# Optimization experiments

Measured on AMD Instinct MI355X. Metric: run time of the kernel, lower is better.

Reference implementation:

```python
import jax, jax.numpy as jnp
import numpy as np
import math

B, S, D, H = 2, 2048, 1024, 16
DH = D // H
PHI = (1 + math.sqrt(5)) / 2

def _carrier_phases(n_heads):
    # DimensionalHeadManager: 7 rungs with weights 1/phi^i, base phases k*pi/7,
    # per-rung heads spread uniformly around the circle.
    base = [k * math.pi / 7 for k in range(7)]
    raw_w = [1.0 / PHI ** i for i in range(7)]
    tw = sum(raw_w)
    alloc = [max(1, round(n_heads * w / tw)) for w in raw_w]
    while sum(alloc) > n_heads:
        alloc[alloc.index(max(alloc))] -= 1
    while sum(alloc) < n_heads:
        alloc[alloc.index(max(alloc))] += 1
    phases = []
    for r, c in enumerate(alloc):
        for j in range(c):
            phases.append(base[r] + 2 * math.pi / max(c, 1) * j)
    return np.array(phases, dtype=np.float32)

def setup_inputs() -> dict:
    key = jax.random.key(0)
    ks = jax.random.split(key, 8)
    x = jax.random.normal(ks[0], (B, S, D), dtype=jnp.float32)
    input_phase = jax.random.uniform(ks[1], (B, S), dtype=jnp.float32) * (2 * math.pi)
    sc = 1.0 / math.sqrt(D)
    Wq = jax.random.normal(ks[2], (D, D), dtype=jnp.float32) * sc
    Wk = jax.random.normal(ks[3], (D, D), dtype=jnp.float32) * sc
    Wv = jax.random.normal(ks[4], (D, D), dtype=jnp.float32) * sc
    Wo = jax.random.normal(ks[5], (D, D), dtype=jnp.float32) * sc
    gamma = jnp.ones((D,), dtype=jnp.float32)
    beta = jnp.zeros((D,), dtype=jnp.float32)
    # per-head fractal compression exponents > 1 (sub-linear for |x|<1)
    exponents = 1.0 + 0.5 * jax.random.uniform(ks[6], (H,), dtype=jnp.float32)
    carrier_phases = jnp.asarray(_carrier_phases(H))
    balance = jnp.asarray(0.5, dtype=jnp.float32)  # BALANCE
    return {"x": x, "input_phase": input_phase, "Wq": Wq, "Wk": Wk, "Wv": Wv,
            "Wo": Wo, "gamma": gamma, "beta": beta, "exponents": exponents,
            "carrier_phases": carrier_phases, "balance": balance}

def _layernorm(x, gamma, beta, eps=1e-5):
    mu = jnp.mean(x, axis=-1, keepdims=True)
    var = jnp.var(x, axis=-1, keepdims=True)
    return (x - mu) * jax.lax.rsqrt(var + eps) * gamma + beta

def _fractal_compress(kv, exps):
    # sign-preserving power-law compression, per-head exponent
    sign = jnp.sign(kv)
    mag = jnp.maximum(jnp.abs(kv), 1e-8)
    return sign * mag ** exps  # exps broadcast (1,H,1,1)

def reference(x, input_phase, Wq, Wk, Wv, Wo, gamma, beta, exponents,
              carrier_phases, balance):
    h = _layernorm(x, gamma, beta)
    def split_heads(t):
        return t.reshape(B, S, H, DH).transpose(0, 2, 1, 3)  # (B,H,S,dh)
    q = split_heads(h @ Wq)
    k = split_heads(h @ Wk)
    v = split_heads(h @ Wv)
    exps = exponents.reshape(1, H, 1, 1)
    k_c = _fractal_compress(k, exps)
    v_c = _fractal_compress(v, exps)
    # per-head carrier resonance: (B,S,H) in [0,1]
    T = jnp.cos((input_phase[:, :, None] - carrier_phases[None, None, :]) / 2.0) ** 2
    Th = T.transpose(0, 2, 1)  # (B,H,S)
    # balance temperature tau = clip(1/(2*balance), 0.1, 10)
    tau = jnp.clip(1.0 / (2.0 * balance + 1e-8), 0.1, 10.0)
    scores = jnp.einsum('bhqd,bhkd->bhqk', q, k_c) / math.sqrt(DH)
    # phase modulation: key-side resonance enters scores in log-space
    scores = scores + jnp.log(Th[:, :, None, :] + 1e-6)
    causal = jnp.tril(jnp.ones((S, S), dtype=bool))
    scores = jnp.where(causal[None, None], scores, jnp.float32(-1e9))
    attn = jax.nn.softmax(scores / tau, axis=-1)
    out = jnp.einsum('bhqk,bhkd->bhqd', attn, v_c)
    # query-side resonance gates the per-head output
    out = out * Th[:, :, :, None]
    out = out.transpose(0, 2, 1, 3).reshape(B, S, D)
    return x + out @ Wo
```

## Files before the change

### kernel.cpp

```cpp
#include <hip/hip_runtime.h>
#include <math.h>

namespace {
constexpr int B = 2, S = 2048, D = 1024, H = 16, DH = 64;
constexpr int BH = B * H;
constexpr int BS = B * S;
constexpr size_t MAT = (size_t)BS * D;
constexpr int QT = S / 64;
}

typedef __attribute__((ext_vector_type(8))) short s16x8;
typedef __attribute__((ext_vector_type(4))) short s16x4;
typedef __attribute__((ext_vector_type(4))) float f32x4;

__device__ inline unsigned short f2bf(float f) {
  union { float f; unsigned u; } c; c.f = f;
  unsigned r = c.u + 0x7fffu + ((c.u >> 16) & 1u);
  return (unsigned short)(r >> 16);
}
__device__ inline short f2bft(float f) {
  union { float f; unsigned u; } c; c.f = f;
  return (short)((c.u + 0x8000u) >> 16);
}
__device__ inline float bf2f(short s) {
  union { unsigned u; float f; } c;
  c.u = ((unsigned)(unsigned short)s) << 16;
  return c.f;
}
__device__ inline void gld16(const unsigned short* g, unsigned short* l) {
  __builtin_amdgcn_global_load_lds(
      (const __attribute__((address_space(1))) unsigned int*)g,
      (__attribute__((address_space(3))) unsigned int*)l, 16, 0, 0);
}

__global__ __launch_bounds__(256) void k_prep(
    const float* __restrict__ x, const float* __restrict__ gamma,
    const float* __restrict__ beta, unsigned short* __restrict__ h,
    const float* __restrict__ phase, const float* __restrict__ cp,
    const float* __restrict__ bal, float* __restrict__ Th,
    float* __restrict__ Lt, const float* __restrict__ W0,
    const float* __restrict__ W1, const float* __restrict__ W2,
    const float* __restrict__ W3, unsigned short* __restrict__ T0,
    unsigned short* __restrict__ T1, unsigned short* __restrict__ T2,
    unsigned short* __restrict__ T3) {
  __shared__ float shbuf[32 * 33];
  int id = blockIdx.x;
  int t = threadIdx.x;
  if (id < 4096) {
    int z = id & 3;
    int bx = ((id >> 2) & 31) * 32;
    int by = (id >> 7) * 32;
    const float* W = (z == 0) ? W0 : (z == 1) ? W1 : (z == 2) ? W2 : W3;
    unsigned short* T = (z == 0) ? T0 : (z == 1) ? T1 : (z == 2) ? T2 : T3;
    int tc = t & 31, tr = t >> 5;
    float(*tile)[33] = (float(*)[33])shbuf;
#pragma unroll
    for (int i = 0; i < 4; i++)
      tile[tr + 8 * i][tc] = W[(size_t)(by + tr + 8 * i) * D + bx + tc];
    __syncthreads();
#pragma unroll
    for (int i = 0; i < 4; i++)
      T[(size_t)(bx + tr + 8 * i) * D + by + tc] = f2bf(tile[tc][tr + 8 * i]);
  } else if (id < 8192) {
    int row = id - 4096;
    float* red = shbuf;
    const float* xr = x + (size_t)row * D;
    float v[4];
    float s = 0.f;
#pragma unroll
    for (int i = 0; i < 4; i++) {
      v[i] = xr[t + 256 * i];
      s += v[i];
    }
    red[t] = s;
    __syncthreads();
    for (int off = 128; off > 0; off >>= 1) {
      if (t < off) red[t] += red[t + off];
      __syncthreads();
    }
    float mu = red[0] * (1.0f / D);
    __syncthreads();
    float s2 = 0.f;
#pragma unroll
    for (int i = 0; i < 4; i++) {
      float d0 = v[i] - mu;
      s2 += d0 * d0;
    }
    red[t] = s2;
    __syncthreads();
    for (int off = 128; off > 0; off >>= 1) {
      if (t < off) red[t] += red[t + off];
      __syncthreads();
    }
    float r = rsqrtf(red[0] * (1.0f / D) + 1e-5f);
    unsigned short* hr = h + (size_t)row * D;
#pragma unroll
    for (int i = 0; i < 4; i++) {
      int c = t + 256 * i;
      hr[c] = f2bf((v[i] - mu) * r * gamma[c] + beta[c]);
    }
  } else {
    int idx = (id - 8192) * 256 + t;
    int s = idx & (S - 1);
    int bh = idx >> 11;
    int hh = bh & (H - 1);
    int b = bh >> 4;
    float tau = fminf(fmaxf(1.0f / (2.0f * bal[0] + 1e-8f), 0.1f), 10.0f);
    float c = cosf((phase[b * S + s] - cp[hh]) * 0.5f);
    float T = c * c;
    Th[idx] = T;
    Lt[idx] = __log2f(T + 1e-6f) * (1.0f / tau);
  }
}

#define MFMA_GEMM_LOOP_TBUF(AP, BP)                                           \
  do {                                                                        \
    gld16(AP, &As[0][chunkA][0]);                                             \
    gld16(AP + (size_t)16 * D, &As[0][chunkA + 16][0]);                       \
    gld16(BP, &Bs[0][chunkA][0]);                                             \
    gld16(BP + (size_t)16 * D, &Bs[0][chunkA + 16][0]);                       \
    gld16(AP + 32, &As[1][chunkA][0]);                                        \
    gld16(AP + (size_t)16 * D + 32, &As[1][chunkA + 16][0]);                  \
    gld16(BP + 32, &Bs[1][chunkA][0]);                                        \
    gld16(BP + (size_t)16 * D + 32, &Bs[1][chunkA + 16][0]);                  \
    int cur = 0;                                                              \
    for (int k0 = 0; k0 < D; k0 += 32) {                                      \
      if (k0 + 32 < D)                                                        \
        asm volatile("s_waitcnt vmcnt(4)" ::: "memory");                      \
      else                                                                    \
        asm volatile("s_waitcnt vmcnt(0)" ::: "memory");                      \
      asm volatile("s_barrier" ::: "memory");                                 \
      if (k0 + 64 < D) {                                                      \
        int nxt = (cur >= 1) ? cur - 1 : 2;                    \
        gld16(AP + k0 + 64, &As[nxt][chunkA][0]);                             \
        gld16(AP + (size_t)16 * D + k0 + 64, &As[nxt][chunkA + 16][0]);       \
        gld16(BP + k0 + 64, &Bs[nxt][chunkA][0]);                             \
        gld16(BP + (size_t)16 * D + k0 + 64, &Bs[nxt][chunkA + 16][0]);       \
      }                                                                       \
      s16x8 af[4], bf[4];                                                     \
      _Pragma("unroll") for (int i = 0; i < 4; i++) {                         \
        af[i] = *(const s16x8*)&As[cur][wm + i * 16 + lane16][quad * 8];      \
        bf[i] = *(const s16x8*)&Bs[cur][wn + i * 16 + lane16][quad * 8];      \
      }                                                                       \
      _Pragma("unroll") for (int i = 0; i < 4; i++)                           \
          _Pragma("unroll") for (int j = 0; j < 4; j++) acc[i][j] =           \
          __builtin_amdgcn_mfma_f32_16x16x32_bf16(af[i], bf[j], acc[i][j],    \
                                                  0, 0, 0);                   \
      cur = (cur == 2) ? 0 : cur + 1;                                         \
    }                                                                         \
  } while (0)

__global__ __launch_bounds__(256) void k_gemm_qkvv(
    const unsigned short* __restrict__ hm, const unsigned short* __restrict__ Wq,
    const unsigned short* __restrict__ Wk, const unsigned short* __restrict__ Wv,
    const float* __restrict__ exps, unsigned short* __restrict__ q,
    unsigned short* __restrict__ kc, unsigned short* __restrict__ vt) {
  __shared__ __align__(16) unsigned short As[3][128][32];
  __shared__ __align__(16) unsigned short Bs[3][128][32];
  int id = blockIdx.x;
  int xcd = id & 7;
  int inner = id >> 3;
  int z = inner >> 5;
  int rem = inner & 31;
  int mt = (xcd >> 1) * 8 + (rem >> 2);
  int nt = (xcd & 1) * 4 + (rem & 3);
  const unsigned short *Ap, *Bp;
  int tileM, tileN;
  if (z < 2) {
    Ap = hm; Bp = (z == 0) ? Wq : Wk;
    tileM = mt * 128; tileN = nt * 128;
  } else {
    Ap = Wv; Bp = hm;
    tileM = nt * 128; tileN = mt * 128;
  }
  int t = threadIdx.x;
  int wave = t >> 6, lane = t & 63, lane16 = lane & 15, quad = lane >> 4;
  int wm = (wave >> 1) * 64, wn = (wave & 1) * 64;
  int chunkA = wave * 32;
  int srow = (lane >> 2), scol = (lane & 3) * 8;
  const unsigned short* aptr = Ap + (size_t)(tileM + chunkA + srow) * D + scol;
  const unsigned short* bptr = Bp + (size_t)(tileN + chunkA + srow) * D + scol;
  f32x4 acc[4][4] = {};
  MFMA_GEMM_LOOP_TBUF(aptr, bptr);
  if (z < 2) {
    unsigned short* __restrict__ outp = (z == 0) ? q : kc;
    float e0 = exps[tileN >> 6];
    float e1 = exps[(tileN >> 6) + 1];
#pragma unroll
    for (int i = 0; i < 4; i++) {
#pragma unroll
      for (int r = 0; r < 4; r++) {
        int row = tileM + wm + i * 16 + quad * 4 + r;
        int b = row >> 11, s = row & (S - 1);
#pragma unroll
        for (int j = 0; j < 4; j++) {
          int cloc = wn + j * 16 + lane16;
          int head = (tileN + cloc) >> 6;
          int dh = cloc & 63;
          float val = acc[i][j][r];
          if (z != 0) {
            float e = (cloc >> 6) ? e1 : e0;
            float sgn = (val > 0.f) ? 1.f : ((val < 0.f) ? -1.f : 0.f);
            float mg = fmaxf(fabsf(val), 1e-8f);
            val = sgn * __expf(e * __logf(mg));
          }
          outp[((size_t)(b * H + head) * S + s) * DH + dh] = f2bf(val);
        }
      }
    }
  } else {
#pragma unroll
    for (int i = 0; i < 4; i++) {
#pragma unroll
      for (int r = 0; r < 4; r++) {
        int m = tileM + wm + i * 16 + quad * 4 + r;
        int head = m >> 6, dh = m & 63;
        float e = exps[head];
#pragma unroll
        for (int j = 0; j < 4; j++) {
          int n = tileN + wn + j * 16 + lane16;
          int b = n >> 11, s = n & (S - 1);
          float val = acc[i][j][r];
          float sgn = (val > 0.f) ? 1.f : ((val < 0.f) ? -1.f : 0.f);
          float mg = fmaxf(fabsf(val), 1e-8f);
          val = sgn * __expf(e * __logf(mg));
          vt[((size_t)(b * H + head) * DH + dh) * S + s] = f2bf(val);
        }
      }
    }
  }
}

__global__ __launch_bounds__(256) void k_gemm_out_mfma(
    const unsigned short* __restrict__ am, const unsigned short* __restrict__ Wt,
    const float* __restrict__ x, float* __restrict__ outp) {
  __shared__ __align__(16) unsigned short As[3][128][32];
  __shared__ __align__(16) unsigned short Bs[3][128][32];
  int id = blockIdx.x;
  int xcd = id & 7;
  int inner = id >> 3;
  int tileM = ((xcd >> 1) * 8 + (inner >> 2)) * 128;
  int tileN = ((xcd & 1) * 4 + (inner & 3)) * 128;
  int t = threadIdx.x;
  int wave = t >> 6, lane = t & 63, lane16 = lane & 15, quad = lane >> 4;
  int wm = (wave >> 1) * 64, wn = (wave & 1) * 64;
  int chunkA = wave * 32;
  int srow = (lane >> 2), scol = (lane & 3) * 8;
  const unsigned short* aptr = am + (size_t)(tileM + chunkA + srow) * D + scol;
  const unsigned short* bptr = Wt + (size_t)(tileN + chunkA + srow) * D + scol;
  f32x4 acc[4][4] = {};
  MFMA_GEMM_LOOP_TBUF(aptr, bptr);
#pragma unroll
  for (int i = 0; i < 4; i++) {
#pragma unroll
    for (int r = 0; r < 4; r++) {
      int row = tileM + wm + i * 16 + quad * 4 + r;
      const float* xr = x + (size_t)row * D;
      float* orow = outp + (size_t)row * D;
#pragma unroll
      for (int j = 0; j < 4; j++) {
        int col = tileN + wn + j * 16 + lane16;
        orow[col] = xr[col] + acc[i][j][r];
      }
    }
  }
}

__global__ __launch_bounds__(256) void k_attn_mfma(
    const unsigned short* __restrict__ q, const unsigned short* __restrict__ kc,
    const unsigned short* __restrict__ vt, const float* __restrict__ Th,
    const float* __restrict__ Lt, const float* __restrict__ bal,
    unsigned short* __restrict__ ao) {
  __shared__ __align__(16) unsigned short Ks[2][64][72];
  __shared__ __align__(16) unsigned short Vs[2][64][72];
  __shared__ __align__(16) unsigned short Pt[4][16][72];
  __shared__ __align__(16) float Lts[2][64];
  int id = blockIdx.x;
  int bh = (id & 7) + 8 * ((id >> 3) & 3);
  int qt = QT - 1 - (id >> 5);
  int t = threadIdx.x;
  int wave = t >> 6, lane = t & 63;
  int lane16 = lane & 15, quad = lane >> 4;
  float tau = fminf(fmaxf(1.0f / (2.0f * bal[0] + 1e-8f), 0.1f), 10.0f);
  float c1 = 0.125f * (1.0f / tau) * 1.44269504f;
  const unsigned short* qb = q + (size_t)bh * S * DH;
  const unsigned short* kb = kc + (size_t)bh * S * DH;
  const unsigned short* vb = vt + (size_t)bh * DH * S;
  const float* Ltb = Lt + (size_t)bh * S;
  int b = bh >> 4, hh = bh & (H - 1);
  int cr = t >> 3, cc = (t & 7) * 8;
  s16x8 nk0, nk1, nv0, nv1;
  float4 nlt;
#define STAGE_LOAD(KT)                                                  \
  do {                                                                  \
    nk0 = *(const s16x8*)(kb + (size_t)((KT) * 64 + cr) * DH + cc);     \
    nk1 = *(const s16x8*)(kb + (size_t)((KT) * 64 + cr + 32) * DH + cc);\
    nv0 = *(const s16x8*)(vb + (size_t)cr * S + (KT) * 64 + cc);        \
    nv1 = *(const s16x8*)(vb + (size_t)(cr + 32) * S + (KT) * 64 + cc); \
    if (t < 16) nlt = ((const float4*)(Ltb + (KT) * 64))[t];            \
  } while (0)
#define STAGE_WRITE(BF)                                                 \
  do {                                                                  \
    *(s16x8*)&Ks[BF][cr][cc] = nk0;                                     \
    *(s16x8*)&Ks[BF][cr + 32][cc] = nk1;                                \
    *(s16x8*)&Vs[BF][cr][cc] = nv0;                                     \
    *(s16x8*)&Vs[BF][cr + 32][cc] = nv1;                                \
    if (t < 16) ((float4*)Lts[BF])[t] = nlt;                            \
  } while (0)
  int qbase = qt * 64 + wave * 16;
  s16x8 qa0, qa1;
  {
    s16x8 r0 = *(const s16x8*)(qb + (size_t)(qbase + lane16) * DH + quad * 8);
    s16x8 r1 =
        *(const s16x8*)(qb + (size_t)(qbase + lane16) * DH + 32 + quad * 8);
#pragma unroll
    for (int i = 0; i < 8; i++) {
      qa0[i] = f2bft(bf2f(r0[i]) * c1);
      qa1[i] = f2bft(bf2f(r1[i]) * c1);
    }
  }
  STAGE_LOAD(0);
  STAGE_WRITE(0);
  __syncthreads();
  f32x4 O[4] = {};
  float lacc = 0.f;
  for (int kt = 0; kt <= qt; kt++) {
    int cur = kt & 1;
    if (kt < qt) STAGE_LOAD(kt + 1);
    bool diag = (kt == qt);
#pragma unroll
    for (int jk = 0; jk < 4; jk++) {
      s16x8 ka0 = *(const s16x8*)&Ks[cur][jk * 16 + lane16][quad * 8];
      s16x8 ka1 = *(const s16x8*)&Ks[cur][jk * 16 + lane16][32 + quad * 8];
      f32x4 st = {};
      st = __builtin_amdgcn_mfma_f32_16x16x32_bf16(ka0, qa0, st, 0, 0, 0);
      st = __builtin_amdgcn_mfma_f32_16x16x32_bf16(ka1, qa1, st, 0, 0, 0);
      float4 ltv = *(const float4*)&Lts[cur][jk * 16 + quad * 4];
      float lt4[4] = {ltv.x, ltv.y, ltv.z, ltv.w};
      s16x4 pk;
#pragma unroll
      for (int r = 0; r < 4; r++) {
        float vv = fminf(st[r] + lt4[r], 126.f);
        float p = exp2f(vv);
        if (diag)
          p = (jk * 16 + quad * 4 + r <= wave * 16 + lane16) ? p : 0.f;
        lacc += p;
        pk[r] = f2bft(p);
      }
      *(s16x4*)&Pt[wave][lane16][jk * 16 + quad * 4] = pk;
    }
    s16x8 pf0 = *(const s16x8*)&Pt[wave][lane16][quad * 8];
    s16x8 pf1 = *(const s16x8*)&Pt[wave][lane16][32 + quad * 8];
#pragma unroll
    for (int d = 0; d < 4; d++) {
      s16x8 av0 = *(const s16x8*)&Vs[cur][d * 16 + lane16][quad * 8];
      s16x8 av1 = *(const s16x8*)&Vs[cur][d * 16 + lane16][32 + quad * 8];
      O[d] = __builtin_amdgcn_mfma_f32_16x16x32_bf16(av0, pf0, O[d], 0, 0, 0);
      O[d] = __builtin_amdgcn_mfma_f32_16x16x32_bf16(av1, pf1, O[d], 0, 0, 0);
    }
    if (kt < qt) STAGE_WRITE(cur ^ 1);
    __syncthreads();
  }
  lacc += __shfl_xor(lacc, 16, 64);
  lacc += __shfl_xor(lacc, 32, 64);
  int qg = qbase + lane16;
  float scl = Th[(size_t)bh * S + qg] / lacc;
  unsigned short* op = ao + (size_t)(b * S + qg) * D + hh * DH;
#pragma unroll
  for (int d = 0; d < 4; d++) {
    s16x4 pk;
#pragma unroll
    for (int r = 0; r < 4; r++) pk[r] = f2bft(O[d][r] * scl);
    *(s16x4*)(op + d * 16 + quad * 4) = pk;
  }
#undef STAGE_LOAD
#undef STAGE_WRITE
}

extern "C" void kernel_launch(void* const* d_in, const int* in_sizes, int n_in,
                              void* d_out, int out_size, void* d_ws,
                              size_t ws_size, hipStream_t stream) {
  const float* x = (const float*)d_in[0];
  const float* phase = (const float*)d_in[1];
  const float* Wq = (const float*)d_in[2];
  const float* Wk = (const float*)d_in[3];
  const float* Wv = (const float*)d_in[4];
  const float* Wo = (const float*)d_in[5];
  const float* gamma = (const float*)d_in[6];
  const float* beta = (const float*)d_in[7];
  const float* exps = (const float*)d_in[8];
  const float* cph = (const float*)d_in[9];
  const float* bal = (const float*)d_in[10];
  float* out = (float*)d_out;

  unsigned short* hbuf = (unsigned short*)d_ws;
  float* Thbuf = (float*)(hbuf + MAT);
  float* Ltbuf = Thbuf + (size_t)BH * S;
  unsigned short* qbuf = (unsigned short*)(Ltbuf + (size_t)BH * S);
  unsigned short* kbuf = qbuf + MAT;
  unsigned short* vtbuf = kbuf + MAT;
  unsigned short* aobuf = vtbuf + MAT;
  unsigned short* wq_t = aobuf + MAT;
  unsigned short* wk_t = wq_t + (size_t)D * D;
  unsigned short* wv_t = wk_t + (size_t)D * D;
  unsigned short* wo_t = wv_t + (size_t)D * D;

  hipLaunchKernelGGL(k_prep, dim3(8448), dim3(256), 0, stream, x, gamma, beta,
                     hbuf, phase, cph, bal, Thbuf, Ltbuf, Wq, Wk, Wv, Wo, wq_t,
                     wk_t, wv_t, wo_t);
  hipLaunchKernelGGL(k_gemm_qkvv, dim3(768), dim3(256), 0, stream, hbuf, wq_t,
                     wk_t, wv_t, exps, qbuf, kbuf, vtbuf);
  hipLaunchKernelGGL(k_attn_mfma, dim3(1024), dim3(256), 0, stream, qbuf,
                     kbuf, vtbuf, Thbuf, Ltbuf, bal, aobuf);
  hipLaunchKernelGGL(k_gemm_out_mfma, dim3(256), dim3(256), 0, stream, aobuf,
                     wo_t, x, out);
}
```

Before: 201.3 us.

## Enlarge QKV GEMM tile to 256x128 with 512-thread blocks

The fused Q/K/V projection GEMM now uses 256x128 output tiles computed by 8 waves per block instead of 128x128 by 4 waves, halving the grid. The main loop is inlined with a triple-buffered LDS pipeline sized for the larger A tile, and each wave loads a smaller share of B. The goal is more reuse of each B tile per block and fewer global loads per FLOP, at the cost of more LDS per block, fewer blocks to spread across CUs, and possibly lower occupancy. The power-law epilogue also switches from exp/log to exp2/log2 intrinsics.

Result: no change. 203.3 us (+1.0%).

```diff
diff --git a/kernel.cpp b/kernel.cpp
--- a/kernel.cpp
+++ b/kernel.cpp
@@ -150,38 +150,72 @@
     }                                                                         \
   } while (0)
 
-__global__ __launch_bounds__(256) void k_gemm_qkvv(
+__global__ __launch_bounds__(512) void k_gemm_qkvv(
     const unsigned short* __restrict__ hm, const unsigned short* __restrict__ Wq,
     const unsigned short* __restrict__ Wk, const unsigned short* __restrict__ Wv,
     const float* __restrict__ exps, unsigned short* __restrict__ q,
     unsigned short* __restrict__ kc, unsigned short* __restrict__ vt) {
-  __shared__ __align__(16) unsigned short As[3][128][32];
+  __shared__ __align__(16) unsigned short As[3][256][32];
   __shared__ __align__(16) unsigned short Bs[3][128][32];
   int id = blockIdx.x;
   int xcd = id & 7;
-  int inner = id >> 3;
-  int z = inner >> 5;
-  int rem = inner & 31;
-  int mt = (xcd >> 1) * 8 + (rem >> 2);
-  int nt = (xcd & 1) * 4 + (rem & 3);
+  int g = id >> 3;
+  int z = g >> 4;
+  int w = g & 15;
   const unsigned short *Ap, *Bp;
   int tileM, tileN;
   if (z < 2) {
     Ap = hm; Bp = (z == 0) ? Wq : Wk;
-    tileM = mt * 128; tileN = nt * 128;
+    tileM = ((xcd >> 1) * 4 + (w >> 2)) * 256;
+    tileN = ((xcd & 1) * 4 + (w & 3)) * 128;
   } else {
     Ap = Wv; Bp = hm;
-    tileM = nt * 128; tileN = mt * 128;
+    tileM = ((xcd & 1) * 2 + (w >> 3)) * 256;
+    tileN = ((xcd >> 1) * 8 + (w & 7)) * 128;
   }
   int t = threadIdx.x;
   int wave = t >> 6, lane = t & 63, lane16 = lane & 15, quad = lane >> 4;
-  int wm = (wave >> 1) * 64, wn = (wave & 1) * 64;
+  int wm = (wave >> 1) * 64;
+  int wn = (wave & 1) * 64;
   int chunkA = wave * 32;
+  int chunkB = wave * 16;
   int srow = (lane >> 2), scol = (lane & 3) * 8;
   const unsigned short* aptr = Ap + (size_t)(tileM + chunkA + srow) * D + scol;
-  const unsigned short* bptr = Bp + (size_t)(tileN + chunkA + srow) * D + scol;
+  const unsigned short* bptr = Bp + (size_t)(tileN + chunkB + srow) * D + scol;
   f32x4 acc[4][4] = {};
-  MFMA_GEMM_LOOP_TBUF(aptr, bptr);
+  gld16(aptr, &As[0][chunkA][0]);
+  gld16(aptr + (size_t)16 * D, &As[0][chunkA + 16][0]);
+  gld16(bptr, &Bs[0][chunkB][0]);
+  gld16(aptr + 32, &As[1][chunkA][0]);
+  gld16(aptr + (size_t)16 * D + 32, &As[1][chunkA + 16][0]);
+  gld16(bptr + 32, &Bs[1][chunkB][0]);
+  int cur = 0;
+  for (int k0 = 0; k0 < D; k0 += 32) {
+    if (k0 + 32 < D)
+      asm volatile("s_waitcnt vmcnt(3)" ::: "memory");
+    else
+      asm volatile("s_waitcnt vmcnt(0)" ::: "memory");
+    asm volatile("s_barrier" ::: "memory");
+    if (k0 + 64 < D) {
+      int nxt = (cur >= 1) ? cur - 1 : 2;
+      gld16(aptr + k0 + 64, &As[nxt][chunkA][0]);
+      gld16(aptr + (size_t)16 * D + k0 + 64, &As[nxt][chunkA + 16][0]);
+      gld16(bptr + k0 + 64, &Bs[nxt][chunkB][0]);
+    }
+    s16x8 af[4], bf[4];
+#pragma unroll
+    for (int i = 0; i < 4; i++) {
+      af[i] = *(const s16x8*)&As[cur][wm + i * 16 + lane16][quad * 8];
+      bf[i] = *(const s16x8*)&Bs[cur][wn + i * 16 + lane16][quad * 8];
+    }
+#pragma unroll
+    for (int i = 0; i < 4; i++)
+#pragma unroll
+      for (int j = 0; j < 4; j++)
+        acc[i][j] = __builtin_amdgcn_mfma_f32_16x16x32_bf16(af[i], bf[j],
+                                                            acc[i][j], 0, 0, 0);
+    cur = (cur == 2) ? 0 : cur + 1;
+  }
   if (z < 2) {
     unsigned short* __restrict__ outp = (z == 0) ? q : kc;
     float e0 = exps[tileN >> 6];
@@ -202,7 +236,7 @@
             float e = (cloc >> 6) ? e1 : e0;
             float sgn = (val > 0.f) ? 1.f : ((val < 0.f) ? -1.f : 0.f);
             float mg = fmaxf(fabsf(val), 1e-8f);
-            val = sgn * __expf(e * __logf(mg));
+            val = sgn * exp2f(e * __log2f(mg));
           }
           outp[((size_t)(b * H + head) * S + s) * DH + dh] = f2bf(val);
         }
@@ -223,7 +257,7 @@
           float val = acc[i][j][r];
           float sgn = (val > 0.f) ? 1.f : ((val < 0.f) ? -1.f : 0.f);
           float mg = fmaxf(fabsf(val), 1e-8f);
-          val = sgn * __expf(e * __logf(mg));
+          val = sgn * exp2f(e * __log2f(mg));
           vt[((size_t)(b * H + head) * DH + dh) * S + s] = f2bf(val);
         }
       }
@@ -408,7 +442,7 @@
   hipLaunchKernelGGL(k_prep, dim3(8448), dim3(256), 0, stream, x, gamma, beta,
                      hbuf, phase, cph, bal, Thbuf, Ltbuf, Wq, Wk, Wv, Wo, wq_t,
                      wk_t, wv_t, wo_t);
-  hipLaunchKernelGGL(k_gemm_qkvv, dim3(768), dim3(256), 0, stream, hbuf, wq_t,
+  hipLaunchKernelGGL(k_gemm_qkvv, dim3(384), dim3(512), 0, stream, hbuf, wq_t,
                      wk_t, wv_t, exps, qbuf, kbuf, vtbuf);
   hipLaunchKernelGGL(k_attn_mfma, dim3(1024), dim3(256), 0, stream, qbuf,
                      kbuf, vtbuf, Thbuf, Ltbuf, bal, aobuf);
```
